# Kernel optimization log

Measured on AMD Instinct MI355X. Metric: run time of the kernel, lower is better.

The kernel has to match this reference:

```python
import jax, jax.numpy as jnp
import numpy as np


def setup_inputs() -> dict:
    key = jax.random.key(0)
    k1, k2, k3 = jax.random.split(key, 3)
    dim = 512
    x = jax.random.normal(k1, (8, dim, 64, 64), dtype=jnp.float32)
    # 1x1 convs with bias=False are channel matmuls: weight[out_ch, in_ch]
    w_qkv = jax.random.normal(k2, (3 * dim, dim), dtype=jnp.float32) * (dim ** -0.5)
    w_out = jax.random.normal(k3, (dim, dim), dtype=jnp.float32) * (dim ** -0.5)
    return {"x": x, "w_qkv": w_qkv, "w_out": w_out}


def reference(x, w_qkv, w_out):
    b, c, h, w = x.shape
    n = h * w
    scale = c ** -0.5
    xf = x.reshape(b, c, n)                          # b c (h w)
    qkv = jnp.einsum('oc,bcn->bon', w_qkv, xf)       # 1x1 conv QKV projection
    q, k, v = jnp.split(qkv, 3, axis=1)              # each [b, c, n]
    score = jnp.einsum('bcq,bck->bqk', q * scale, k) # full N x N attention
    attn = jax.nn.softmax(score, axis=-1)
    out = jnp.einsum('bqk,bck->bcq', attn, v)        # [b, c, n]
    out = jnp.einsum('oc,bcn->bon', w_out, out)      # 1x1 conv out projection
    return out.reshape(b, c, h, w)
```

## Files before the change

kernel.cpp:

```cpp
#include <hip/hip_runtime.h>
#include <hip/hip_bf16.h>


typedef __bf16 bf16x8 __attribute__((ext_vector_type(8)));
typedef float f32x4 __attribute__((ext_vector_type(4)));
typedef __hip_bfloat16 bf16_t;

static __device__ __forceinline__ void glds16(const void* g, void* l) {
  __builtin_amdgcn_global_load_lds(
      (__attribute__((address_space(1))) const void*)g,
      (__attribute__((address_space(3))) void*)l, 16, 0, 0);
}

#define BAR asm volatile("s_barrier" ::: "memory")
#define LGKM0 asm volatile("s_waitcnt lgkmcnt(0)" ::: "memory")
#define LGKM8 asm volatile("s_waitcnt lgkmcnt(8)" ::: "memory")
#define VM0 asm volatile("s_waitcnt vmcnt(0)" ::: "memory")
#define VM2 asm volatile("s_waitcnt vmcnt(2)" ::: "memory")

#define READ_A(buf, qm)                                                       \
  {                                                                           \
    const int rgA = (((buf)*2 + wm) << 14);                                   \
    _Pragma("unroll") for (int j = 0; j < 4; ++j) {                           \
      const int ro = rgA + ((((qm)*4 + j)*16 + lr) << 7);                     \
      _Pragma("unroll") for (int kk = 0; kk < 2; ++kk)                        \
        av[j][kk] = *(const bf16x8*)(lds + ro + ((kk*64 + lk*16) ^ swz));     \
    }                                                                         \
  }
#define READ_B(buf, qn)                                                       \
  {                                                                           \
    const int rgB = 65536 + (((buf)*2 + bh) << 14) + bsub;                    \
    _Pragma("unroll") for (int n = 0; n < 2; ++n) {                           \
      const int ro = rgB + ((((qn)*2 + n)*16 + lr) << 7);                     \
      _Pragma("unroll") for (int kk = 0; kk < 2; ++kk)                        \
        bv[n][kk] = *(const bf16x8*)(lds + ro + ((kk*64 + lk*16) ^ swz));     \
    }                                                                         \
  }
#define MFMA_Q(qm, qn)                                                        \
  __builtin_amdgcn_s_setprio(1);                                              \
  _Pragma("unroll") for (int j = 0; j < 4; ++j)                               \
    _Pragma("unroll") for (int n = 0; n < 2; ++n)                             \
      _Pragma("unroll") for (int kk = 0; kk < 2; ++kk)                        \
        acc[(qm)*4 + j][(qn)*2 + n] =                                         \
            __builtin_amdgcn_mfma_f32_16x16x32_bf16(                          \
                av[j][kk], bv[n][kk], acc[(qm)*4 + j][(qn)*2 + n], 0, 0, 0);  \
  __builtin_amdgcn_s_setprio(0);

template <int MODE>
__global__ void __launch_bounds__(512, 2)
gemm8(const bf16_t* __restrict__ A, long long strideA, int lda,
      const bf16_t* __restrict__ Bt, long long strideB, int ldb,
      void* __restrict__ Cv, long long strideC, int ldc,
      int K, float scale, float* __restrict__ rowsum, int strideRS) {
  __shared__ char lds[131072];
  const int tid = threadIdx.x;
  const int lane = tid & 63;
  const int wid = tid >> 6;
  const int wm = wid >> 2, wn = wid & 3;
  const int lr = lane & 15, lk = lane >> 4;
  const int swz = (lr & 7) << 4;
  const int bh = wn >> 1, bsub = (wn & 1) << 13;
  const int b = blockIdx.z;

  const char* Ab = (const char*)(A + (long long)b*strideA + (size_t)blockIdx.x*256*lda);
  const char* Bb = (const char*)(Bt + (long long)b*strideB + (size_t)blockIdx.y*256*ldb);
  const size_t ldab = (size_t)lda*2, ldbb = (size_t)ldb*2;

  auto stage = [&](int m, int buf, int half, int kt) {
    const char* src = m ? Bb : Ab;
    const size_t ld = m ? ldbb : ldab;
    char* dst = lds + (m << 16) + ((buf*2 + half) << 14);
#pragma unroll
    for (int c = 0; c < 2; ++c) {
      const int oin = wid*2048 + c*1024 + lane*16;
      const int row = half*128 + (oin >> 7);
      const int kb = (oin & 127) ^ (((oin >> 7) & 7) << 4);
      glds16(src + (size_t)row*ld + (size_t)kt*128 + kb, dst + wid*2048 + c*1024);
    }
  };

  f32x4 acc[8][4] = {};
  bf16x8 av[4][2], bv[2][2];
  const int niter = K >> 7;

  stage(0,0,0,0); stage(0,0,1,0); stage(1,0,0,0); stage(1,0,1,0);
  stage(0,1,0,1);
  VM2; BAR;

  for (int i = 0; i < niter; ++i) {
    const bool nl = (i + 1 < niter);
    const int o1 = 2*i + 1, e2 = 2*i + 2, o3 = 2*i + 3;
    READ_A(0,0); READ_B(0,0); stage(0,1,1,o1);
    LGKM8; BAR; LGKM0; MFMA_Q(0,0); BAR;
    READ_B(0,1); stage(1,1,0,o1);
    BAR; LGKM0; MFMA_Q(0,1); BAR;
    READ_A(0,1); stage(1,1,1,o1);
    BAR; LGKM0; MFMA_Q(1,1); BAR;
    READ_B(0,0); if (nl) stage(0,0,0,e2);
    BAR; LGKM0; MFMA_Q(1,0);
    if (nl) { VM2; } else { VM0; }
    BAR;
    READ_A(1,0); READ_B(1,0); if (nl) stage(0,0,1,e2);
    LGKM8; BAR; LGKM0; MFMA_Q(0,0); BAR;
    READ_B(1,1); if (nl) stage(1,0,0,e2);
    BAR; LGKM0; MFMA_Q(0,1); BAR;
    READ_A(1,1); if (nl) stage(1,0,1,e2);
    BAR; LGKM0; MFMA_Q(1,1); BAR;
    READ_B(1,0); if (nl) stage(0,1,0,o3);
    BAR; LGKM0; MFMA_Q(1,0);
    if (nl) { VM2; }
    BAR;
  }

  const int mbase = blockIdx.x*256 + wm*128;
  const int nbase = blockIdx.y*256 + wn*64;

  if (MODE == 0) {
    bf16_t* C = (bf16_t*)Cv + (long long)b * strideC;
#pragma unroll
    for (int fm = 0; fm < 8; ++fm)
#pragma unroll
      for (int fn = 0; fn < 4; ++fn)
#pragma unroll
        for (int r = 0; r < 4; ++r) {
          const int row = mbase + fm*16 + lk*4 + r;
          const int col = nbase + fn*16 + lr;
          C[(size_t)row*ldc + col] = __float2bfloat16(acc[fm][fn][r]);
        }
  } else if (MODE == 2) {
    bf16_t* P = (bf16_t*)Cv + (long long)b * strideC;
    float* rs = rowsum + (long long)b * strideRS;
#pragma unroll
    for (int fm = 0; fm < 8; ++fm)
#pragma unroll
      for (int r = 0; r < 4; ++r) {
        const int row = mbase + fm*16 + lk*4 + r;
        float s = 0.f;
#pragma unroll
        for (int fn = 0; fn < 4; ++fn) {
          const float v = __expf(acc[fm][fn][r] * scale);
          const int col = nbase + fn*16 + lr;
          P[(size_t)row*ldc + col] = __float2bfloat16(v);
          s += v;
        }
        s += __shfl_xor(s, 1);
        s += __shfl_xor(s, 2);
        s += __shfl_xor(s, 4);
        s += __shfl_xor(s, 8);
        if (lr == 0) atomicAdd(&rs[row], s);
      }
  } else {
    float* O = (float*)Cv + (long long)b * strideC;
    const float* rs = rowsum + (long long)b * strideRS;
#pragma unroll
    for (int fn = 0; fn < 4; ++fn) {
      const int col = nbase + fn*16 + lr;
      const float inv = 1.0f / rs[col];
#pragma unroll
      for (int fm = 0; fm < 8; ++fm)
#pragma unroll
        for (int r = 0; r < 4; ++r) {
          const int row = mbase + fm*16 + lk*4 + r;
          O[(size_t)row*ldc + col] = acc[fm][fn][r] * inv;
        }
    }
  }
}

__global__ void cast_f32_bf16(const float* __restrict__ in, bf16_t* __restrict__ out, int n) {
  const int i = blockIdx.x * blockDim.x + threadIdx.x;
  if (i < n) out[i] = __float2bfloat16(in[i]);
}

__global__ void zero_f32(float* __restrict__ p, int n) {
  const int i = blockIdx.x * blockDim.x + threadIdx.x;
  if (i < n) p[i] = 0.f;
}

__global__ void transpose_cast(const float* __restrict__ x, bf16_t* __restrict__ xT) {
  __shared__ float t[32][33];
  const int b = blockIdx.z;
  const int n0 = blockIdx.x * 32, c0 = blockIdx.y * 32;
  const int tx = threadIdx.x & 31, ty = threadIdx.x >> 5;
  const float* xb = x + (size_t)b * (512 * 4096);
#pragma unroll
  for (int i = 0; i < 32; i += 8)
    t[ty + i][tx] = xb[(size_t)(c0 + ty + i) * 4096 + n0 + tx];
  __syncthreads();
  bf16_t* xo = xT + (size_t)b * (4096 * 512);
#pragma unroll
  for (int i = 0; i < 32; i += 8)
    xo[(size_t)(n0 + ty + i) * 512 + c0 + tx] = __float2bfloat16(t[tx][ty + i]);
}

__global__ void transpose_cast_512(const float* __restrict__ in, bf16_t* __restrict__ out) {
  __shared__ float t[32][33];
  const int r0 = blockIdx.x * 32, c0 = blockIdx.y * 32;
  const int tx = threadIdx.x & 31, ty = threadIdx.x >> 5;
#pragma unroll
  for (int i = 0; i < 32; i += 8)
    t[ty + i][tx] = in[(size_t)(r0 + ty + i) * 512 + c0 + tx];
  __syncthreads();
#pragma unroll
  for (int i = 0; i < 32; i += 8)
    out[(size_t)(c0 + ty + i) * 512 + r0 + tx] = __float2bfloat16(t[tx][ty + i]);
}

extern "C" void kernel_launch(void* const* d_in, const int* in_sizes, int n_in,
                              void* d_out, int out_size, void* d_ws, size_t ws_size,
                              hipStream_t stream) {
  const float* x = (const float*)d_in[0];
  const float* wqkv = (const float*)d_in[1];
  const float* wout = (const float*)d_in[2];
  char* ws = (char*)d_ws;

  const size_t o_qkT = 0;
  const size_t o_U   = 67108864ull;
  const size_t o_wqk = 100663296ull;
  const size_t o_wo  = 101711872ull;
  const size_t o_wvT = 102236160ull;
  const size_t o_wov = 102760448ull;
  const size_t o_rs  = 103284736ull;
  const size_t o_xT  = 103415808ull;

  bf16_t* qkT  = (bf16_t*)(ws + o_qkT);
  bf16_t* U    = (bf16_t*)(ws + o_U);
  bf16_t* wqkb = (bf16_t*)(ws + o_wqk);
  bf16_t* wob  = (bf16_t*)(ws + o_wo);
  bf16_t* wvT  = (bf16_t*)(ws + o_wvT);
  bf16_t* wov  = (bf16_t*)(ws + o_wov);
  float*  rs   = (float*)(ws + o_rs);
  bf16_t* xT   = (bf16_t*)(ws + o_xT);
  bf16_t* P    = (bf16_t*)(ws + o_xT);

  const size_t pbytes = 33554432ull;
  const size_t avail = ws_size > o_xT ? ws_size - o_xT : 0;
  int chunk = 1;
  if (avail >= 8 * pbytes) chunk = 8;
  else if (avail >= 4 * pbytes) chunk = 4;
  else if (avail >= 2 * pbytes) chunk = 2;

  const float scale = 0.04419417382415922f;

  cast_f32_bf16<<<2048, 256, 0, stream>>>(wqkv, wqkb, 524288);
  cast_f32_bf16<<<1024, 256, 0, stream>>>(wout, wob, 262144);
  transpose_cast_512<<<dim3(16, 16), 256, 0, stream>>>(wqkv + 524288, wvT);
  zero_f32<<<128, 256, 0, stream>>>(rs, 32768);
  transpose_cast<<<dim3(128, 16, 8), 256, 0, stream>>>(x, xT);

  gemm8<0><<<dim3(16, 4, 8), 512, 0, stream>>>(
      xT, 2097152LL, 512, wqkb, 0LL, 512, qkT, 4194304LL, 1024, 512, 1.f, nullptr, 0);

  gemm8<0><<<dim3(2, 2, 1), 512, 0, stream>>>(
      wob, 0LL, 512, wvT, 0LL, 512, wov, 0LL, 512, 512, 1.f, nullptr, 0);

  gemm8<0><<<dim3(2, 16, 8), 512, 0, stream>>>(
      wov, 0LL, 512, xT, 2097152LL, 512, U, 2097152LL, 4096, 512, 1.f, nullptr, 0);

  for (int cb = 0; cb < 8; cb += chunk) {
    gemm8<2><<<dim3(16, 16, chunk), 512, 0, stream>>>(
        qkT + (size_t)cb * 4194304, 4194304LL, 1024,
        qkT + (size_t)cb * 4194304 + 512, 4194304LL, 1024,
        P, 16777216LL, 4096, 512, scale, rs + cb * 4096, 4096);
    gemm8<5><<<dim3(2, 16, chunk), 512, 0, stream>>>(
        U + (size_t)cb * 2097152, 2097152LL, 4096,
        P, 16777216LL, 4096,
        (float*)d_out + (size_t)cb * 2097152, 2097152LL, 4096,
        4096, 1.f, rs + cb * 4096, 4096);
  }
}
```

Measured before the change: 636.9 us.

## Split-K the attention-value GEMM with atomic output and restage LDS loads

The final P·V GEMM (MODE 5) now splits its K=4096 reduction into two halves across blockIdx.z. This doubles the grid from 256 to 512 blocks to improve CU occupancy, and the halves are combined with float atomicAdd into an output that is zeroed beforehand. The GEMM main loop is also reorganised: each thread issues one 16-byte global-to-LDS load per 64-row slice, LDS uses a contiguous per-buffer layout, and the schedule changes to 16-MFMA groups with double B fragments and a deeper vmcnt(6) prefetch window. The cost is atomic write traffic on the output, an extra zeroing pass, and non-deterministic summation order.

```diff
diff --git a/kernel.cpp b/kernel.cpp
--- a/kernel.cpp
+++ b/kernel.cpp
@@ -14,39 +14,31 @@
 
 #define BAR asm volatile("s_barrier" ::: "memory")
 #define LGKM0 asm volatile("s_waitcnt lgkmcnt(0)" ::: "memory")
-#define LGKM8 asm volatile("s_waitcnt lgkmcnt(8)" ::: "memory")
 #define VM0 asm volatile("s_waitcnt vmcnt(0)" ::: "memory")
-#define VM2 asm volatile("s_waitcnt vmcnt(2)" ::: "memory")
-
-#define READ_A(buf, qm)                                                       \
-  {                                                                           \
-    const int rgA = (((buf)*2 + wm) << 14);                                   \
-    _Pragma("unroll") for (int j = 0; j < 4; ++j) {                           \
-      const int ro = rgA + ((((qm)*4 + j)*16 + lr) << 7);                     \
-      _Pragma("unroll") for (int kk = 0; kk < 2; ++kk)                        \
-        av[j][kk] = *(const bf16x8*)(lds + ro + ((kk*64 + lk*16) ^ swz));     \
-    }                                                                         \
-  }
-#define READ_B(buf, qn)                                                       \
-  {                                                                           \
-    const int rgB = 65536 + (((buf)*2 + bh) << 14) + bsub;                    \
-    _Pragma("unroll") for (int n = 0; n < 2; ++n) {                           \
-      const int ro = rgB + ((((qn)*2 + n)*16 + lr) << 7);                     \
-      _Pragma("unroll") for (int kk = 0; kk < 2; ++kk)                        \
-        bv[n][kk] = *(const bf16x8*)(lds + ro + ((kk*64 + lk*16) ^ swz));     \
-    }                                                                         \
-  }
-#define MFMA_Q(qm, qn)                                                        \
-  __builtin_amdgcn_s_setprio(1);                                              \
-  _Pragma("unroll") for (int j = 0; j < 4; ++j)                               \
-    _Pragma("unroll") for (int n = 0; n < 2; ++n)                             \
-      _Pragma("unroll") for (int kk = 0; kk < 2; ++kk)                        \
-        acc[(qm)*4 + j][(qn)*2 + n] =                                         \
-            __builtin_amdgcn_mfma_f32_16x16x32_bf16(                          \
-                av[j][kk], bv[n][kk], acc[(qm)*4 + j][(qn)*2 + n], 0, 0, 0);  \
+#define VM6 asm volatile("s_waitcnt vmcnt(6)" ::: "memory")
+
+#define RD_A(buf, fb)                                                       \
+  _Pragma("unroll") for (int j = 0; j < 4; ++j)                             \
+    _Pragma("unroll") for (int kk = 0; kk < 2; ++kk)                        \
+      avr[j][kk] = *(const bf16x8*)(lds + (buf)*32768 +                     \
+          ((wm*128 + ((fb)+j)*16 + lr) << 7) + ((kk*64 + lk*16) ^ swz));
+
+#define RD_B(dst, buf, fb)                                                  \
+  _Pragma("unroll") for (int n = 0; n < 2; ++n)                             \
+    _Pragma("unroll") for (int kk = 0; kk < 2; ++kk)                        \
+      dst[n][kk] = *(const bf16x8*)(lds + 65536 + (buf)*32768 +             \
+          ((wn*64 + ((fb)+n)*16 + lr) << 7) + ((kk*64 + lk*16) ^ swz));
+
+#define MFMA16(bvx, fb, nb)                                                 \
+  __builtin_amdgcn_s_setprio(1);                                            \
+  _Pragma("unroll") for (int j = 0; j < 4; ++j)                             \
+    _Pragma("unroll") for (int n = 0; n < 2; ++n)                           \
+      _Pragma("unroll") for (int kk = 0; kk < 2; ++kk)                      \
+        acc[(fb)+j][(nb)+n] = __builtin_amdgcn_mfma_f32_16x16x32_bf16(      \
+            avr[j][kk], bvx[n][kk], acc[(fb)+j][(nb)+n], 0, 0, 0);          \
   __builtin_amdgcn_s_setprio(0);
 
-template <int MODE>
+template <int MODE, int KSPLIT>
 __global__ void __launch_bounds__(512, 2)
 gemm8(const bf16_t* __restrict__ A, long long strideA, int lda,
       const bf16_t* __restrict__ Bt, long long strideB, int ldb,
@@ -59,56 +51,62 @@
   const int wm = wid >> 2, wn = wid & 3;
   const int lr = lane & 15, lk = lane >> 4;
   const int swz = (lr & 7) << 4;
-  const int bh = wn >> 1, bsub = (wn & 1) << 13;
-  const int b = blockIdx.z;
-
-  const char* Ab = (const char*)(A + (long long)b*strideA + (size_t)blockIdx.x*256*lda);
-  const char* Bb = (const char*)(Bt + (long long)b*strideB + (size_t)blockIdx.y*256*ldb);
+  const int rowl = tid >> 3;
+  const int kbl = ((tid * 16) & 127) ^ ((rowl & 7) << 4);
+
+  int b = blockIdx.z, ks = 0;
+  if (KSPLIT) { ks = b & 1; b >>= 1; }
+  const bf16_t* Ap = A + (size_t)ks * K;
+  const bf16_t* Btp = Bt + (size_t)ks * K;
+
+  const char* Ab = (const char*)(Ap + (long long)b*strideA + (size_t)blockIdx.x*256*lda);
+  const char* Bb = (const char*)(Btp + (long long)b*strideB + (size_t)blockIdx.y*256*ldb);
   const size_t ldab = (size_t)lda*2, ldbb = (size_t)ldb*2;
 
-  auto stage = [&](int m, int buf, int half, int kt) {
-    const char* src = m ? Bb : Ab;
-    const size_t ld = m ? ldbb : ldab;
-    char* dst = lds + (m << 16) + ((buf*2 + half) << 14);
-#pragma unroll
-    for (int c = 0; c < 2; ++c) {
-      const int oin = wid*2048 + c*1024 + lane*16;
-      const int row = half*128 + (oin >> 7);
-      const int kb = (oin & 127) ^ (((oin >> 7) & 7) << 4);
-      glds16(src + (size_t)row*ld + (size_t)kt*128 + kb, dst + wid*2048 + c*1024);
-    }
+  auto stage = [&](int m, int buf, int u, int kt) {
+    const char* src = (m ? Bb : Ab) + (size_t)(u*64 + rowl) * (m ? ldbb : ldab)
+                      + (size_t)kt*128 + kbl;
+    glds16(src, lds + m*65536 + buf*32768 + u*8192 + wid*1024);
   };
 
   f32x4 acc[8][4] = {};
-  bf16x8 av[4][2], bv[2][2];
+  bf16x8 avr[4][2], bva[2][2], bvb[2][2];
   const int niter = K >> 7;
 
-  stage(0,0,0,0); stage(0,0,1,0); stage(1,0,0,0); stage(1,0,1,0);
-  stage(0,1,0,1);
-  VM2; BAR;
+  stage(0,0,0,0); stage(0,0,1,0); stage(0,0,2,0); stage(0,0,3,0);
+  stage(1,0,0,0); stage(1,0,1,0); stage(1,0,2,0); stage(1,0,3,0);
+  stage(0,1,0,1); stage(0,1,2,1);
+  stage(1,1,0,1); stage(1,1,1,1); stage(1,1,2,1); stage(1,1,3,1);
+  VM6; BAR;
 
   for (int i = 0; i < niter; ++i) {
     const bool nl = (i + 1 < niter);
-    const int o1 = 2*i + 1, e2 = 2*i + 2, o3 = 2*i + 3;
-    READ_A(0,0); READ_B(0,0); stage(0,1,1,o1);
-    LGKM8; BAR; LGKM0; MFMA_Q(0,0); BAR;
-    READ_B(0,1); stage(1,1,0,o1);
-    BAR; LGKM0; MFMA_Q(0,1); BAR;
-    READ_A(0,1); stage(1,1,1,o1);
-    BAR; LGKM0; MFMA_Q(1,1); BAR;
-    READ_B(0,0); if (nl) stage(0,0,0,e2);
-    BAR; LGKM0; MFMA_Q(1,0);
-    if (nl) { VM2; } else { VM0; }
+    const int ko = 2*i + 1, ke2 = 2*i + 2, ko3 = 2*i + 3;
+    stage(0,1,1,ko); stage(0,1,3,ko);
+    RD_A(0,0); RD_B(bva,0,0);
+    MFMA16(bva, 0, 0); LGKM0; BAR;
+    if (nl) { stage(0,0,0,ke2); stage(0,0,2,ke2); }
+    RD_B(bvb,0,2);
+    MFMA16(bvb, 0, 2); LGKM0; BAR;
+    if (nl) { stage(1,0,0,ke2); stage(1,0,1,ke2); }
+    RD_A(0,4);
+    MFMA16(bvb, 4, 2); LGKM0; BAR;
+    if (nl) { stage(1,0,2,ke2); stage(1,0,3,ke2); }
+    MFMA16(bva, 4, 0);
+    if (nl) { VM6; } else { VM0; }
     BAR;
-    READ_A(1,0); READ_B(1,0); if (nl) stage(0,0,1,e2);
-    LGKM8; BAR; LGKM0; MFMA_Q(0,0); BAR;
-    READ_B(1,1); if (nl) stage(1,0,0,e2);
-    BAR; LGKM0; MFMA_Q(0,1); BAR;
-    READ_A(1,1); if (nl) stage(1,0,1,e2);
-    BAR; LGKM0; MFMA_Q(1,1); BAR;
-    READ_B(1,0); if (nl) stage(0,1,0,o3);
-    BAR; LGKM0; MFMA_Q(1,0);
-    if (nl) { VM2; }
+    if (nl) { stage(0,0,1,ke2); stage(0,0,3,ke2); }
+    RD_A(1,0); RD_B(bva,1,0);
+    MFMA16(bva, 0, 0); LGKM0; BAR;
+    if (nl) { stage(0,1,0,ko3); stage(0,1,2,ko3); }
+    RD_B(bvb,1,2);
+    MFMA16(bvb, 0, 2); LGKM0; BAR;
+    if (nl) { stage(1,1,0,ko3); stage(1,1,1,ko3); }
+    RD_A(1,4);
+    MFMA16(bvb, 4, 2); LGKM0; BAR;
+    if (nl) { stage(1,1,2,ko3); stage(1,1,3,ko3); }
+    MFMA16(bva, 4, 0);
+    if (nl) { VM6; }
     BAR;
   }
 
@@ -161,7 +159,7 @@
 #pragma unroll
         for (int r = 0; r < 4; ++r) {
           const int row = mbase + fm*16 + lk*4 + r;
-          O[(size_t)row*ldc + col] = acc[fm][fn][r] * inv;
+          atomicAdd(&O[(size_t)row*ldc + col], acc[fm][fn][r] * inv);
         }
     }
   }
@@ -173,8 +171,8 @@
 }
 
 __global__ void zero_f32(float* __restrict__ p, int n) {
-  const int i = blockIdx.x * blockDim.x + threadIdx.x;
-  if (i < n) p[i] = 0.f;
+  for (int i = blockIdx.x * blockDim.x + threadIdx.x; i < n; i += gridDim.x * blockDim.x)
+    p[i] = 0.f;
 }
 
 __global__ void transpose_cast(const float* __restrict__ x, bf16_t* __restrict__ xT) {
@@ -246,26 +244,27 @@
   cast_f32_bf16<<<1024, 256, 0, stream>>>(wout, wob, 262144);
   transpose_cast_512<<<dim3(16, 16), 256, 0, stream>>>(wqkv + 524288, wvT);
   zero_f32<<<128, 256, 0, stream>>>(rs, 32768);
+  zero_f32<<<2048, 256, 0, stream>>>((float*)d_out, out_size);
   transpose_cast<<<dim3(128, 16, 8), 256, 0, stream>>>(x, xT);
 
-  gemm8<0><<<dim3(16, 4, 8), 512, 0, stream>>>(
+  gemm8<0,0><<<dim3(16, 4, 8), 512, 0, stream>>>(
       xT, 2097152LL, 512, wqkb, 0LL, 512, qkT, 4194304LL, 1024, 512, 1.f, nullptr, 0);
 
-  gemm8<0><<<dim3(2, 2, 1), 512, 0, stream>>>(
+  gemm8<0,0><<<dim3(2, 2, 1), 512, 0, stream>>>(
       wob, 0LL, 512, wvT, 0LL, 512, wov, 0LL, 512, 512, 1.f, nullptr, 0);
 
-  gemm8<0><<<dim3(2, 16, 8), 512, 0, stream>>>(
+  gemm8<0,0><<<dim3(2, 16, 8), 512, 0, stream>>>(
       wov, 0LL, 512, xT, 2097152LL, 512, U, 2097152LL, 4096, 512, 1.f, nullptr, 0);
 
   for (int cb = 0; cb < 8; cb += chunk) {
-    gemm8<2><<<dim3(16, 16, chunk), 512, 0, stream>>>(
+    gemm8<2,0><<<dim3(16, 16, chunk), 512, 0, stream>>>(
         qkT + (size_t)cb * 4194304, 4194304LL, 1024,
         qkT + (size_t)cb * 4194304 + 512, 4194304LL, 1024,
         P, 16777216LL, 4096, 512, scale, rs + cb * 4096, 4096);
-    gemm8<5><<<dim3(2, 16, chunk), 512, 0, stream>>>(
+    gemm8<5,1><<<dim3(2, 16, chunk * 2), 512, 0, stream>>>(
         U + (size_t)cb * 2097152, 2097152LL, 4096,
         P, 16777216LL, 4096,
         (float*)d_out + (size_t)cb * 2097152, 2097152LL, 4096,
-        4096, 1.f, rs + cb * 4096, 4096);
+        2048, 1.f, rs + cb * 4096, 4096);
   }
 }
```

Measured after the change: 621.5 us. 1.02x faster.
